# Kernel optimization log

Measured on AMD Instinct MI355X. Metric: run time of the kernel, lower is better.

## Reference

```python
import math
import jax, jax.numpy as jnp
import numpy as np

B, I, D, H, K, MAXI, FF = 2, 1024, 1024, 16, 64, 1024, 4096
DH = D // H
EPS = 1e-5

def _ln(x, g, b):
    m = x.mean(-1, keepdims=True)
    v = ((x - m) ** 2).mean(-1, keepdims=True)
    return (x - m) / jnp.sqrt(v + EPS) * g + b

def setup_inputs() -> dict:
    key = jax.random.key(0)
    ks = jax.random.split(key, 16)
    p = lambda i, sh: (0.02 * jax.random.normal(ks[i], sh)).astype(jnp.float32)
    # clamped relative-position indices: clamp(j - floor(1.0*i), -K, K) + K
    ar = np.arange(MAXI)
    idx = np.clip(ar[None, :] - ar[:, None], -K, K) + K  # [maxI, maxI]
    return {
        'x': jax.random.normal(ks[0], (B, I, D), dtype=jnp.float32),
        'j': jax.random.normal(ks[1], (B, I, D), dtype=jnp.float32),
        'ln1_g': jnp.ones((D,), jnp.float32), 'ln1_b': jnp.zeros((D,), jnp.float32),
        'Wv_w': p(2, (D, D)), 'Wv_b': jnp.zeros((D,), jnp.float32),
        'Wg_w': p(3, (D, D)), 'Wg_b': jnp.zeros((D,), jnp.float32),
        'lnv_g': jnp.ones((D,), jnp.float32), 'lnv_b': jnp.zeros((D,), jnp.float32),
        'Wq1_w': p(4, (D, D)), 'Wq1_b': jnp.zeros((D,), jnp.float32),
        'Wk_w': p(5, (D, D)), 'Wk_b': jnp.zeros((D,), jnp.float32),
        'Wq2_w': p(6, (D, D)), 'Wq2_b': jnp.zeros((D,), jnp.float32),
        'rel_emb': p(7, (2 * K + 1, D)),
        'Wo_w': p(8, (D, D)), 'Wo_b': jnp.zeros((D,), jnp.float32),
        'ln2_g': jnp.ones((D,), jnp.float32), 'ln2_b': jnp.zeros((D,), jnp.float32),
        'ff1_w': p(9, (D, FF)), 'ff1_b': jnp.zeros((FF,), jnp.float32),
        'ff2_w': p(10, (FF, D)), 'ff2_b': jnp.zeros((D,), jnp.float32),
        'indices': jnp.asarray(idx, jnp.int32),
    }

def reference(x, j, ln1_g, ln1_b, Wv_w, Wv_b, Wg_w, Wg_b, lnv_g, lnv_b,
              Wq1_w, Wq1_b, Wk_w, Wk_b, Wq2_w, Wq2_b, rel_emb,
              Wo_w, Wo_b, ln2_g, ln2_b, ff1_w, ff1_b, ff2_w, ff2_b, indices):
    Bv, Iq, _ = x.shape
    res = x
    xn = _ln(x, ln1_g, ln1_b)
    # value / gate streams with gelu activation, layernorm on v only
    v = _ln(jax.nn.gelu(xn @ Wv_w + Wv_b, approximate=False), lnv_g, lnv_b)
    g = jax.nn.gelu(xn @ Wg_w + Wg_b, approximate=False)
    vh = v.reshape(Bv, -1, H, DH)   # [B,J,H,Dh]
    gh = g.reshape(Bv, -1, H, DH)   # [B,I,H,Dh]
    # absolute-position scores: Q1(j) . K(j)^T
    q1 = (j @ Wq1_w + Wq1_b).reshape(Bv, -1, H, DH)
    kh = (j @ Wk_w + Wk_b).reshape(Bv, -1, H, DH)
    aa = jnp.einsum('bihd,bjhd->bhij', q1, kh)  # [B,H,I,J]
    # relative-position scores: Q2(j) . rel_embed^T, gathered by clamped indices
    q2 = (j @ Wq2_w + Wq2_b).reshape(Bv, -1, H, DH)
    rh = rel_emb.reshape(2 * K + 1, H, DH)
    arf = jnp.einsum('bihd,rhd->bhir', q2, rh)  # [B,H,I,2K+1]
    Jk = kh.shape[1]
    idx = jnp.broadcast_to(indices[None, None, :Iq, :Jk], (Bv, H, Iq, Jk))
    ar = jnp.take_along_axis(arf, idx, axis=-1)  # [B,H,I,J]
    a = jax.nn.softmax((aa + ar) / math.sqrt(DH), axis=-1)
    o = jnp.einsum('bhij,bjhd->bihd', a, vh) * gh  # gated attention output
    o = o.reshape(Bv, -1, D) @ Wo_w + Wo_b
    x1 = o + res
    # feed-forward sublayer
    h = jax.nn.relu(_ln(x1, ln2_g, ln2_b) @ ff1_w + ff1_b)
    out = h @ ff2_w + ff2_b + x1
    return (out, a)
```

## Files before the change

kernel.cpp:

```cpp
#include <hip/hip_runtime.h>
#include <hip/hip_bf16.h>
#include <math.h>

#define D_   1024
#define H_   16
#define DH_  64
#define FF_  4096
#define R_   129
#define I_   1024
#define B_   2
#define MROWS 2048
#define QKVLD 3072

typedef __bf16 v8bf16 __attribute__((ext_vector_type(8)));
typedef float f32x4 __attribute__((ext_vector_type(4)));

__device__ __forceinline__ float gelu_f(float x) {
    return 0.5f * x * (1.0f + erff(x * 0.7071067811865476f));
}

__device__ __forceinline__ void ldsld16(const void* g, void* l) {
    __builtin_amdgcn_global_load_lds(
        (const __attribute__((address_space(1))) void*)g,
        (__attribute__((address_space(3))) void*)l, 16, 0, 0);
}

__global__ __launch_bounds__(256) void cvt_bf16(const float* __restrict__ in,
        __hip_bfloat16* __restrict__ out, int n4) {
    int i = blockIdx.x * 256 + threadIdx.x;
    if (i >= n4) return;
    float4 v = reinterpret_cast<const float4*>(in)[i];
    union { __hip_bfloat16 h[4]; uint2 u; } pk;
    pk.h[0] = __float2bfloat16(v.x); pk.h[1] = __float2bfloat16(v.y);
    pk.h[2] = __float2bfloat16(v.z); pk.h[3] = __float2bfloat16(v.w);
    reinterpret_cast<uint2*>(out)[i] = pk.u;
}

__global__ __launch_bounds__(256) void wtrans(const float* __restrict__ W,
        __hip_bfloat16* __restrict__ WT, int K, int N) {
    __shared__ float T[64][65];
    int k0 = blockIdx.y * 64, n0 = blockIdx.x * 64;
    int t = threadIdx.x;
#pragma unroll
    for (int i = 0; i < 16; i++) {
        int e = t + i * 256, r = e >> 6, c = e & 63;
        T[r][c] = W[(size_t)(k0 + r) * N + n0 + c];
    }
    __syncthreads();
#pragma unroll
    for (int i = 0; i < 16; i++) {
        int e = t + i * 256, r = e >> 6, c = e & 63;
        WT[(size_t)(n0 + r) * K + k0 + c] = __float2bfloat16(T[c][r]);
    }
}

__global__ __launch_bounds__(256) void wtrans6(
        const float* __restrict__ s0, const float* __restrict__ s1,
        const float* __restrict__ s2, const float* __restrict__ s3,
        const float* __restrict__ s4, const float* __restrict__ s5,
        __hip_bfloat16* __restrict__ d0, __hip_bfloat16* __restrict__ d1,
        __hip_bfloat16* __restrict__ d2, __hip_bfloat16* __restrict__ d3,
        __hip_bfloat16* __restrict__ d4, __hip_bfloat16* __restrict__ d5) {
    __shared__ float T[64][65];
    int z = blockIdx.z;
    const float* W = z == 0 ? s0 : z == 1 ? s1 : z == 2 ? s2 : z == 3 ? s3 : z == 4 ? s4 : s5;
    __hip_bfloat16* WT = z == 0 ? d0 : z == 1 ? d1 : z == 2 ? d2 : z == 3 ? d3 : z == 4 ? d4 : d5;
    int k0 = blockIdx.y * 64, n0 = blockIdx.x * 64;
    int t = threadIdx.x;
#pragma unroll
    for (int i = 0; i < 16; i++) {
        int e = t + i * 256, r = e >> 6, c = e & 63;
        T[r][c] = W[(size_t)(k0 + r) * D_ + n0 + c];
    }
    __syncthreads();
#pragma unroll
    for (int i = 0; i < 16; i++) {
        int e = t + i * 256, r = e >> 6, c = e & 63;
        WT[(size_t)(n0 + r) * D_ + k0 + c] = __float2bfloat16(T[c][r]);
    }
}

__global__ __launch_bounds__(256) void vtrans(const float* __restrict__ v,
        __hip_bfloat16* __restrict__ vt) {
    __shared__ float T[64][65];
    int z = blockIdx.y, b = z >> 4, h = z & 15;
    int j0 = blockIdx.x * 64;
    int t = threadIdx.x;
#pragma unroll
    for (int i = 0; i < 16; i++) {
        int e = t + i * 256, r = e >> 6, c = e & 63;
        T[r][c] = v[(size_t)(b * I_ + j0 + r) * D_ + h * DH_ + c];
    }
    __syncthreads();
#pragma unroll
    for (int i = 0; i < 16; i++) {
        int e = t + i * 256, r = e >> 6, c = e & 63;
        vt[((size_t)z * DH_ + r) * I_ + j0 + c] = __float2bfloat16(T[c][r]);
    }
}

template<int MR, int NWC, int ACT, int RES, int OUTBF>
__global__ __launch_bounds__(256) void gemm_mfma(
        const __hip_bfloat16* __restrict__ A,
        const __hip_bfloat16* __restrict__ Bt,
        const float* __restrict__ bias,
        const float* __restrict__ res,
        void* __restrict__ Cout,
        int N, int Kd, int lda, int ldb, int ldc,
        size_t sAb, size_t sAh, size_t sBb, size_t sBh, size_t sCz) {
    constexpr int NWR = 4 / NWC;
    constexpr int BM = NWR * MR * 16;
    constexpr int BN = NWC * 64;
    __shared__ __align__(16) __hip_bfloat16 As[BM * 64];
    __shared__ __align__(16) __hip_bfloat16 Bs[BN * 64];
    const char* AsB = (const char*)As;
    const char* BsB = (const char*)Bs;
    int z = blockIdx.z;
    const __hip_bfloat16* Ab = A + (size_t)(z >> 4) * sAb + (size_t)(z & 15) * sAh;
    const __hip_bfloat16* Bb = Bt + (size_t)(z >> 4) * sBb + (size_t)(z & 15) * sBh;
    float* Cf = (float*)Cout + (size_t)z * sCz;
    __hip_bfloat16* Cb = (__hip_bfloat16*)Cout + (size_t)z * sCz;
    int m0 = blockIdx.y * BM, n0 = blockIdx.x * BN;
    int t = threadIdx.x;
    int l = t & 63, w = t >> 6;
    int wr = w / NWC, wc = w % NWC;
    int lr = l & 15, kq = l >> 4;
    int rx = lr & 7;

    f32x4 acc[MR][4] = {};

    for (int k0 = 0; k0 < Kd; k0 += 64) {
#pragma unroll
        for (int i = 0; i < BM / 32; i++) {
            int e = t + i * 256;
            int row = e >> 3, sl = e & 7;
            int kb = sl ^ (row & 7);
            ldsld16(Ab + (size_t)(m0 + row) * lda + (k0 + kb * 8), (void*)(AsB + e * 16));
        }
#pragma unroll
        for (int i = 0; i < BN / 32; i++) {
            int e = t + i * 256;
            int row = e >> 3, sl = e & 7;
            int kb = sl ^ (row & 7);
            int nr = n0 + row; if (nr > N - 1) nr = N - 1;
            ldsld16(Bb + (size_t)nr * ldb + (k0 + kb * 8), (void*)(BsB + e * 16));
        }
        __syncthreads();
#pragma unroll
        for (int kc = 0; kc < 2; kc++) {
            int sloff = (((kc << 2) + kq) ^ rx) << 4;
            v8bf16 af[MR], bfr[4];
#pragma unroll
            for (int mr = 0; mr < MR; mr++)
                af[mr] = *(const v8bf16*)(AsB + ((wr * (MR * 16) + mr * 16 + lr) << 7) + sloff);
#pragma unroll
            for (int nc = 0; nc < 4; nc++)
                bfr[nc] = *(const v8bf16*)(BsB + ((wc * 64 + nc * 16 + lr) << 7) + sloff);
#pragma unroll
            for (int mr = 0; mr < MR; mr++)
#pragma unroll
                for (int nc = 0; nc < 4; nc++)
                    acc[mr][nc] = __builtin_amdgcn_mfma_f32_16x16x32_bf16(
                        af[mr], bfr[nc], acc[mr][nc], 0, 0, 0);
        }
        __syncthreads();
    }

#pragma unroll
    for (int mr = 0; mr < MR; mr++) {
        int rbase = m0 + wr * (MR * 16) + mr * 16 + kq * 4;
#pragma unroll
        for (int nc = 0; nc < 4; nc++) {
            int col = n0 + wc * 64 + nc * 16 + lr;
            bool okc = col < N;
            float bv = (bias && okc) ? bias[col] : 0.f;
#pragma unroll
            for (int ri = 0; ri < 4; ri++) {
                int r = rbase + ri;
                float val = acc[mr][nc][ri] + bv;
                if (ACT == 1) val = gelu_f(val);
                if (ACT == 2) val = fmaxf(val, 0.f);
                if (RES) val += res[(size_t)r * ldc + col];
                if (okc) {
                    if (OUTBF == 2) {
                        if (col < D_) Cf[(size_t)r * ldc + col] = val;
                        else ((__hip_bfloat16*)res)[(size_t)r * ldc + (col - D_)] =
                                 __float2bfloat16(val);
                    } else if (OUTBF == 1) {
                        Cb[(size_t)r * ldc + col] = __float2bfloat16(val);
                    } else {
                        Cf[(size_t)r * ldc + col] = val;
                    }
                }
            }
        }
    }
}

#define FA_AR 0
#define FA_K  16896
#define FA_V  (16896 + 8192)
#define FA_P  (16896 + 16384)
#define SC2   0.1803368801111244f
__global__ __launch_bounds__(256) void flash_attn3(
        const __hip_bfloat16* __restrict__ qkv,
        const __hip_bfloat16* __restrict__ vt,
        const __hip_bfloat16* __restrict__ arfb,
        const __hip_bfloat16* __restrict__ gb,
        float* __restrict__ a_out,
        __hip_bfloat16* __restrict__ obuf) {
    __shared__ __align__(16) char lds[16896 + 8192 * 3];
    __hip_bfloat16* arl = (__hip_bfloat16*)(lds + FA_AR);
    char* kB = lds + FA_K;
    char* vB = lds + FA_V;
    char* pB = lds + FA_P;

    int z = blockIdx.y, b = z >> 4, h = z & 15;
    int i0 = blockIdx.x * 64;
    int t = threadIdx.x, l = t & 63, w = t >> 6;
    int lr = l & 15, kq = l >> 4;

#pragma unroll
    for (int i = 0; i < 2; i++) {
        int e = t + i * 256;
        int row = e >> 3, sl = e & 7;
        int kb = sl ^ (row & 7);
        ldsld16(qkv + (size_t)(b * I_ + i0 + row) * QKVLD + h * DH_ + kb * 8,
                (void*)(pB + e * 16));
    }
    for (int idx = t; idx < 64 * 132; idx += 256) {
        int row = idx / 132, r = idx - row * 132;
        if (r < R_) arl[idx] = arfb[((size_t)z * I_ + i0 + row) * R_ + r];
    }
    __syncthreads();
    v8bf16 qf[2];
#pragma unroll
    for (int kc = 0; kc < 2; kc++)
        qf[kc] = *(const v8bf16*)(pB + ((w * 16 + lr) << 7) + ((((kc << 2) + kq) ^ (lr & 7)) << 4));

    int irow = w * 16 + kq * 4;
    int ig = i0 + irow;
    float loS[4], hiS[4];
#pragma unroll
    for (int ri = 0; ri < 4; ri++) {
        loS[ri] = __bfloat162float(arl[(irow + ri) * 132 + 0])   * SC2;
        hiS[ri] = __bfloat162float(arl[(irow + ri) * 132 + 128]) * SC2;
    }

    float l_ln[4] = {0.f, 0.f, 0.f, 0.f};
    for (int jt = 0; jt < 16; jt++) {
        int j0 = jt * 64;
#pragma unroll
        for (int i = 0; i < 2; i++) {
            int e = t + i * 256;
            int row = e >> 3, sl = e & 7;
            int kb = sl ^ (row & 7);
            ldsld16(qkv + (size_t)(b * I_ + j0 + row) * QKVLD + D_ + h * DH_ + kb * 8,
                    (void*)(kB + e * 16));
        }
        __syncthreads();
        f32x4 acc[4] = {};
        __builtin_amdgcn_s_setprio(1);
#pragma unroll
        for (int kc = 0; kc < 2; kc++) {
            int sloff = ((((kc << 2) + kq)) ^ (lr & 7)) << 4;
#pragma unroll
            for (int tt = 0; tt < 4; tt++) {
                v8bf16 kf = *(const v8bf16*)(kB + ((tt * 16 + lr) << 7) + sloff);
                acc[tt] = __builtin_amdgcn_mfma_f32_16x16x32_bf16(qf[kc], kf, acc[tt], 0, 0, 0);
            }
        }
        __builtin_amdgcn_s_setprio(0);
#pragma unroll
        for (int ri = 0; ri < 4; ri++) {
            int i_g = ig + ri;
            float sc[4];
            bool lo_all = (j0 + 63) <= (i_g - 64);
            bool hi_all = j0 >= (i_g + 64);
            if (lo_all || hi_all) {
                float c = lo_all ? loS[ri] : hiS[ri];
#pragma unroll
                for (int tt = 0; tt < 4; tt++) sc[tt] = fmaf(acc[tt][ri], SC2, c);
            } else {
#pragma unroll
                for (int tt = 0; tt < 4; tt++) {
                    int rel = j0 + tt * 16 + lr - i_g;
                    rel = rel < -64 ? -64 : (rel > 64 ? 64 : rel);
                    sc[tt] = (acc[tt][ri] + __bfloat162float(arl[(irow + ri) * 132 + rel + 64])) * SC2;
                }
            }
            l_ln[ri] += exp2f(sc[0]) + exp2f(sc[1]) + exp2f(sc[2]) + exp2f(sc[3]);
        }
        __syncthreads();
    }
    float offb[4];
#pragma unroll
    for (int ri = 0; ri < 4; ri++) {
        float s = l_ln[ri];
#pragma unroll
        for (int off = 1; off < 16; off <<= 1) s += __shfl_xor(s, off, 64);
        offb[ri] = __log2f(s);
    }

    f32x4 oacc[4] = {};
    for (int jt = 0; jt < 16; jt++) {
        int j0 = jt * 64;
#pragma unroll
        for (int i = 0; i < 2; i++) {
            int e = t + i * 256;
            int row = e >> 3, sl = e & 7;
            int kb = sl ^ (row & 7);
            ldsld16(qkv + (size_t)(b * I_ + j0 + row) * QKVLD + D_ + h * DH_ + kb * 8,
                    (void*)(kB + e * 16));
            ldsld16(vt + ((size_t)z * DH_ + row) * I_ + j0 + kb * 8,
                    (void*)(vB + e * 16));
        }
        __syncthreads();
        f32x4 acc[4] = {};
        __builtin_amdgcn_s_setprio(1);
#pragma unroll
        for (int kc = 0; kc < 2; kc++) {
            int sloff = ((((kc << 2) + kq)) ^ (lr & 7)) << 4;
#pragma unroll
            for (int tt = 0; tt < 4; tt++) {
                v8bf16 kf = *(const v8bf16*)(kB + ((tt * 16 + lr) << 7) + sloff);
                acc[tt] = __builtin_amdgcn_mfma_f32_16x16x32_bf16(qf[kc], kf, acc[tt], 0, 0, 0);
            }
        }
        __builtin_amdgcn_s_setprio(0);
#pragma unroll
        for (int ri = 0; ri < 4; ri++) {
            int i_g = ig + ri;
            int rowl = irow + ri;
            float sc[4];
            bool lo_all = (j0 + 63) <= (i_g - 64);
            bool hi_all = j0 >= (i_g + 64);
            if (lo_all || hi_all) {
                float c = lo_all ? loS[ri] : hiS[ri];
#pragma unroll
                for (int tt = 0; tt < 4; tt++) sc[tt] = fmaf(acc[tt][ri], SC2, c);
            } else {
#pragma unroll
                for (int tt = 0; tt < 4; tt++) {
                    int rel = j0 + tt * 16 + lr - i_g;
                    rel = rel < -64 ? -64 : (rel > 64 ? 64 : rel);
                    sc[tt] = (acc[tt][ri] + __bfloat162float(arl[rowl * 132 + rel + 64])) * SC2;
                }
            }
            float* gout = a_out + ((size_t)z * I_ + i0 + rowl) * I_ + j0;
#pragma unroll
            for (int tt = 0; tt < 4; tt++) {
                float p = exp2f(sc[tt] - offb[ri]);
                __builtin_nontemporal_store(p, gout + tt * 16 + lr);
                *(__hip_bfloat16*)(pB + (rowl << 7) +
                        ((((tt * 2) + (lr >> 3)) ^ (rowl & 7)) << 4) + (lr & 7) * 2) =
                    __float2bfloat16(p);
            }
        }
        __syncthreads();
        __builtin_amdgcn_s_setprio(1);
#pragma unroll
        for (int kc = 0; kc < 2; kc++) {
            int sloff = ((((kc << 2) + kq)) ^ (lr & 7)) << 4;
            v8bf16 pf = *(const v8bf16*)(pB + ((w * 16 + lr) << 7) + sloff);
#pragma unroll
            for (int nc = 0; nc < 4; nc++) {
                v8bf16 vf = *(const v8bf16*)(vB + ((nc * 16 + lr) << 7) + sloff);
                oacc[nc] = __builtin_amdgcn_mfma_f32_16x16x32_bf16(pf, vf, oacc[nc], 0, 0, 0);
            }
        }
        __builtin_amdgcn_s_setprio(0);
        __syncthreads();
    }
#pragma unroll
    for (int nc = 0; nc < 4; nc++) {
#pragma unroll
        for (int ri = 0; ri < 4; ri++) {
            int r = i0 + irow + ri;
            size_t oi = ((size_t)(b * I_ + r)) * D_ + h * DH_ + nc * 16 + lr;
            obuf[oi] = __float2bfloat16(oacc[nc][ri] * __bfloat162float(gb[oi]));
        }
    }
}

template<int OUTBF>
__global__ __launch_bounds__(256) void ln_kernel(const float* __restrict__ in,
        void* __restrict__ out, const float* __restrict__ gw,
        const float* __restrict__ bw) {
    __shared__ float shs[4], shq[4];
    int row = blockIdx.x;
    int t = threadIdx.x;
    float4 v = reinterpret_cast<const float4*>(in + (size_t)row * D_)[t];
    float s = v.x + v.y + v.z + v.w;
#pragma unroll
    for (int off = 32; off > 0; off >>= 1) s += __shfl_down(s, off, 64);
    if ((t & 63) == 0) shs[t >> 6] = s;
    __syncthreads();
    float mean = (shs[0] + shs[1] + shs[2] + shs[3]) * (1.0f / D_);
    float d0 = v.x - mean, d1 = v.y - mean, d2 = v.z - mean, d3 = v.w - mean;
    float q = d0 * d0 + d1 * d1 + d2 * d2 + d3 * d3;
#pragma unroll
    for (int off = 32; off > 0; off >>= 1) q += __shfl_down(q, off, 64);
    if ((t & 63) == 0) shq[t >> 6] = q;
    __syncthreads();
    float var = (shq[0] + shq[1] + shq[2] + shq[3]) * (1.0f / D_);
    float rstd = rsqrtf(var + 1e-5f);
    float4 g4 = reinterpret_cast<const float4*>(gw)[t];
    float4 b4 = reinterpret_cast<const float4*>(bw)[t];
    float o0 = d0 * rstd * g4.x + b4.x;
    float o1 = d1 * rstd * g4.y + b4.y;
    float o2 = d2 * rstd * g4.z + b4.z;
    float o3 = d3 * rstd * g4.w + b4.w;
    if (OUTBF) {
        union { __hip_bfloat16 h[4]; uint2 u; } pk;
        pk.h[0] = __float2bfloat16(o0); pk.h[1] = __float2bfloat16(o1);
        pk.h[2] = __float2bfloat16(o2); pk.h[3] = __float2bfloat16(o3);
        reinterpret_cast<uint2*>((__hip_bfloat16*)out + (size_t)row * D_)[t] = pk.u;
    } else {
        float4 o; o.x = o0; o.y = o1; o.z = o2; o.w = o3;
        reinterpret_cast<float4*>((float*)out + (size_t)row * D_)[t] = o;
    }
}

extern "C" void kernel_launch(void* const* d_in, const int* in_sizes, int n_in,
                              void* d_out, int out_size, void* d_ws, size_t ws_size,
                              hipStream_t stream) {
    const float* x      = (const float*)d_in[0];
    const float* jin    = (const float*)d_in[1];
    const float* ln1_g  = (const float*)d_in[2];
    const float* ln1_b  = (const float*)d_in[3];
    const float* Wv_w   = (const float*)d_in[4];
    const float* Wv_b   = (const float*)d_in[5];
    const float* Wg_w   = (const float*)d_in[6];
    const float* Wg_b   = (const float*)d_in[7];
    const float* lnv_g  = (const float*)d_in[8];
    const float* lnv_b  = (const float*)d_in[9];
    const float* Wq1_w  = (const float*)d_in[10];
    const float* Wq1_b  = (const float*)d_in[11];
    const float* Wk_w   = (const float*)d_in[12];
    const float* Wk_b   = (const float*)d_in[13];
    const float* Wq2_w  = (const float*)d_in[14];
    const float* Wq2_b  = (const float*)d_in[15];
    const float* rel    = (const float*)d_in[16];
    const float* Wo_w   = (const float*)d_in[17];
    const float* Wo_b   = (const float*)d_in[18];
    const float* ln2_g  = (const float*)d_in[19];
    const float* ln2_b  = (const float*)d_in[20];
    const float* ff1_w  = (const float*)d_in[21];
    const float* ff1_b  = (const float*)d_in[22];
    const float* ff2_w  = (const float*)d_in[23];
    const float* ff2_b  = (const float*)d_in[24];

    float* out0  = (float*)d_out;
    float* a_out = out0 + (size_t)B_ * I_ * D_;

    char* wsb = (char*)d_ws;
    const size_t MB = 1u << 20;
    __hip_bfloat16* wvwgT= (__hip_bfloat16*)(wsb + 0 * MB);
    __hip_bfloat16* qkvT = (__hip_bfloat16*)(wsb + 4 * MB);
    __hip_bfloat16* WoT  = (__hip_bfloat16*)(wsb + 10 * MB);
    __hip_bfloat16* ff1T = (__hip_bfloat16*)(wsb + 12 * MB);
    __hip_bfloat16* ff2T = (__hip_bfloat16*)(wsb + 20 * MB);
    __hip_bfloat16* jbf  = (__hip_bfloat16*)(wsb + 28 * MB);
    __hip_bfloat16* qkv  = (__hip_bfloat16*)(wsb + 32 * MB);
    __hip_bfloat16* relb = (__hip_bfloat16*)(wsb + 44 * MB);
    __hip_bfloat16* arfb = (__hip_bfloat16*)(wsb + 45 * MB);
    __hip_bfloat16* gbuf = (__hip_bfloat16*)(wsb + 54 * MB);
    float*          vbuf = (float*)        (wsb + 58 * MB);
    __hip_bfloat16* xnb  = (__hip_bfloat16*)(wsb + 28 * MB);
    __hip_bfloat16* vt   = (__hip_bfloat16*)(wsb + 28 * MB);
    __hip_bfloat16* obuf = (__hip_bfloat16*)(wsb + 58 * MB);
    float*          x1   = (float*)        (wsb + 32 * MB);
    __hip_bfloat16* x1nb = (__hip_bfloat16*)(wsb + 40 * MB);
    __hip_bfloat16* hbuf = (__hip_bfloat16*)(wsb + 44 * MB);
    float*          bias3= (float*)        (wsb + 66 * MB);
    float*          bias2= (float*)        (wsb + 66 * MB + 16384);

    dim3 blk(256);

    cvt_bf16<<<2048, blk, 0, stream>>>(jin, jbf, (MROWS * D_) / 4);
    cvt_bf16<<<129, blk, 0, stream>>>(rel, relb, (R_ * D_) / 4);
    hipMemcpyAsync(bias3,        Wq1_b, D_ * 4, hipMemcpyDeviceToDevice, stream);
    hipMemcpyAsync(bias3 + D_,   Wk_b,  D_ * 4, hipMemcpyDeviceToDevice, stream);
    hipMemcpyAsync(bias3 + 2*D_, Wq2_b, D_ * 4, hipMemcpyDeviceToDevice, stream);
    hipMemcpyAsync(bias2,        Wv_b,  D_ * 4, hipMemcpyDeviceToDevice, stream);
    hipMemcpyAsync(bias2 + D_,   Wg_b,  D_ * 4, hipMemcpyDeviceToDevice, stream);
    wtrans6<<<dim3(16, 16, 6), blk, 0, stream>>>(
        Wq1_w, Wk_w, Wq2_w, Wv_w, Wg_w, Wo_w,
        qkvT, qkvT + 1024*1024, qkvT + 2048*1024,
        wvwgT, wvwgT + 1024*1024, WoT);
    wtrans<<<dim3(64, 16), blk, 0, stream>>>(ff1_w, ff1T, D_, FF_);
    wtrans<<<dim3(16, 64), blk, 0, stream>>>(ff2_w, ff2T, FF_, D_);

    gemm_mfma<2, 2, 0, 0, 1><<<dim3(24, 32, 1), blk, 0, stream>>>(
        jbf, qkvT, bias3, nullptr, qkv, QKVLD, D_, D_, D_, QKVLD, 0, 0, 0, 0, 0);
    gemm_mfma<4, 2, 0, 0, 1><<<dim3(2, 8, 32), blk, 0, stream>>>(
        qkv + 2 * D_, relb, nullptr, nullptr, arfb,
        R_, DH_, QKVLD, D_, R_,
        (size_t)I_ * QKVLD, (size_t)DH_, 0, (size_t)DH_, (size_t)I_ * R_);

    ln_kernel<1><<<MROWS, blk, 0, stream>>>(x, xnb, ln1_g, ln1_b);
    gemm_mfma<2, 2, 1, 0, 2><<<dim3(16, 32, 1), blk, 0, stream>>>(
        xnb, wvwgT, bias2, (const float*)gbuf, vbuf, 2 * D_, D_, D_, D_, D_, 0, 0, 0, 0, 0);
    ln_kernel<0><<<MROWS, blk, 0, stream>>>(vbuf, vbuf, lnv_g, lnv_b);
    vtrans<<<dim3(16, 32), blk, 0, stream>>>(vbuf, vt);

    flash_attn3<<<dim3(16, 32), blk, 0, stream>>>(qkv, vt, arfb, gbuf, a_out, obuf);

    gemm_mfma<2, 1, 0, 1, 0><<<dim3(16, 16, 1), blk, 0, stream>>>(
        obuf, WoT, Wo_b, x, x1, D_, D_, D_, D_, D_, 0, 0, 0, 0, 0);
    ln_kernel<1><<<MROWS, blk, 0, stream>>>(x1, x1nb, ln2_g, ln2_b);
    gemm_mfma<4, 2, 2, 0, 1><<<dim3(32, 16, 1), blk, 0, stream>>>(
        x1nb, ff1T, ff1_b, nullptr, hbuf, FF_, D_, D_, D_, FF_, 0, 0, 0, 0, 0);
    gemm_mfma<2, 1, 0, 1, 0><<<dim3(16, 16, 1), blk, 0, stream>>>(
        hbuf, ff2T, ff2_b, x1, out0, D_, FF_, FF_, FF_, D_, 0, 0, 0, 0, 0);
}
```

Before: 281.1 us.

## Merge small setup launches and enlarge M-tiles for QKV and value/gate GEMMs

Replaces the rel_emb conversion and five bias memcpys with one combined kernel, and merges the two FF weight transposes into a single launch. This cuts the number of launches and memcpy operations. It also switches the QKV and value/gate GEMMs to a taller M tile (4 instead of 2) with half as many row blocks, which improves operand reuse but leaves fewer workgroups to fill the CUs.

```diff
diff --git a/kernel.cpp b/kernel.cpp
--- a/kernel.cpp
+++ b/kernel.cpp
@@ -36,21 +36,25 @@
     reinterpret_cast<uint2*>(out)[i] = pk.u;
 }
 
-__global__ __launch_bounds__(256) void wtrans(const float* __restrict__ W,
-        __hip_bfloat16* __restrict__ WT, int K, int N) {
-    __shared__ float T[64][65];
-    int k0 = blockIdx.y * 64, n0 = blockIdx.x * 64;
-    int t = threadIdx.x;
-#pragma unroll
-    for (int i = 0; i < 16; i++) {
-        int e = t + i * 256, r = e >> 6, c = e & 63;
-        T[r][c] = W[(size_t)(k0 + r) * N + n0 + c];
-    }
-    __syncthreads();
-#pragma unroll
-    for (int i = 0; i < 16; i++) {
-        int e = t + i * 256, r = e >> 6, c = e & 63;
-        WT[(size_t)(n0 + r) * K + k0 + c] = __float2bfloat16(T[c][r]);
+__global__ __launch_bounds__(256) void cvt_rel_bias(const float* __restrict__ rel,
+        __hip_bfloat16* __restrict__ relb,
+        const float* __restrict__ q1b_, const float* __restrict__ kb_,
+        const float* __restrict__ q2b_, const float* __restrict__ vb_,
+        const float* __restrict__ gb_,
+        float* __restrict__ bias3, float* __restrict__ bias2) {
+    int bid = blockIdx.x, t = threadIdx.x;
+    if (bid < 129) {
+        int i = bid * 256 + t;
+        float4 v = reinterpret_cast<const float4*>(rel)[i];
+        union { __hip_bfloat16 h[4]; uint2 u; } pk;
+        pk.h[0] = __float2bfloat16(v.x); pk.h[1] = __float2bfloat16(v.y);
+        pk.h[2] = __float2bfloat16(v.z); pk.h[3] = __float2bfloat16(v.w);
+        reinterpret_cast<uint2*>(relb)[i] = pk.u;
+    } else {
+        int k = bid - 129;
+        const float* src = k == 0 ? q1b_ : k == 1 ? kb_ : k == 2 ? q2b_ : k == 3 ? vb_ : gb_;
+        float* dst = (k < 3 ? bias3 + k * D_ : bias2 + (k - 3) * D_);
+        reinterpret_cast<float4*>(dst)[t] = reinterpret_cast<const float4*>(src)[t];
     }
 }
 
@@ -77,6 +81,31 @@
     for (int i = 0; i < 16; i++) {
         int e = t + i * 256, r = e >> 6, c = e & 63;
         WT[(size_t)(n0 + r) * D_ + k0 + c] = __float2bfloat16(T[c][r]);
+    }
+}
+
+__global__ __launch_bounds__(256) void wtrans_ff(
+        const float* __restrict__ f1, const float* __restrict__ f2,
+        __hip_bfloat16* __restrict__ d1, __hip_bfloat16* __restrict__ d2) {
+    __shared__ float T[64][65];
+    int z = blockIdx.z;
+    const float* W = z == 0 ? f1 : f2;
+    __hip_bfloat16* WT = z == 0 ? d1 : d2;
+    int K = z == 0 ? D_ : FF_;
+    int N = z == 0 ? FF_ : D_;
+    int k0 = (z == 0 ? blockIdx.y : blockIdx.x) * 64;
+    int n0 = (z == 0 ? blockIdx.x : blockIdx.y) * 64;
+    int t = threadIdx.x;
+#pragma unroll
+    for (int i = 0; i < 16; i++) {
+        int e = t + i * 256, r = e >> 6, c = e & 63;
+        T[r][c] = W[(size_t)(k0 + r) * N + n0 + c];
+    }
+    __syncthreads();
+#pragma unroll
+    for (int i = 0; i < 16; i++) {
+        int e = t + i * 256, r = e >> 6, c = e & 63;
+        WT[(size_t)(n0 + r) * K + k0 + c] = __float2bfloat16(T[c][r]);
     }
 }
 
@@ -479,20 +508,15 @@
     dim3 blk(256);
 
     cvt_bf16<<<2048, blk, 0, stream>>>(jin, jbf, (MROWS * D_) / 4);
-    cvt_bf16<<<129, blk, 0, stream>>>(rel, relb, (R_ * D_) / 4);
-    hipMemcpyAsync(bias3,        Wq1_b, D_ * 4, hipMemcpyDeviceToDevice, stream);
-    hipMemcpyAsync(bias3 + D_,   Wk_b,  D_ * 4, hipMemcpyDeviceToDevice, stream);
-    hipMemcpyAsync(bias3 + 2*D_, Wq2_b, D_ * 4, hipMemcpyDeviceToDevice, stream);
-    hipMemcpyAsync(bias2,        Wv_b,  D_ * 4, hipMemcpyDeviceToDevice, stream);
-    hipMemcpyAsync(bias2 + D_,   Wg_b,  D_ * 4, hipMemcpyDeviceToDevice, stream);
+    cvt_rel_bias<<<134, blk, 0, stream>>>(rel, relb,
+        Wq1_b, Wk_b, Wq2_b, Wv_b, Wg_b, bias3, bias2);
     wtrans6<<<dim3(16, 16, 6), blk, 0, stream>>>(
         Wq1_w, Wk_w, Wq2_w, Wv_w, Wg_w, Wo_w,
         qkvT, qkvT + 1024*1024, qkvT + 2048*1024,
         wvwgT, wvwgT + 1024*1024, WoT);
-    wtrans<<<dim3(64, 16), blk, 0, stream>>>(ff1_w, ff1T, D_, FF_);
-    wtrans<<<dim3(16, 64), blk, 0, stream>>>(ff2_w, ff2T, FF_, D_);
-
-    gemm_mfma<2, 2, 0, 0, 1><<<dim3(24, 32, 1), blk, 0, stream>>>(
+    wtrans_ff<<<dim3(64, 16, 2), blk, 0, stream>>>(ff1_w, ff2_w, ff1T, ff2T);
+
+    gemm_mfma<4, 2, 0, 0, 1><<<dim3(24, 16, 1), blk, 0, stream>>>(
         jbf, qkvT, bias3, nullptr, qkv, QKVLD, D_, D_, D_, QKVLD, 0, 0, 0, 0, 0);
     gemm_mfma<4, 2, 0, 0, 1><<<dim3(2, 8, 32), blk, 0, stream>>>(
         qkv + 2 * D_, relb, nullptr, nullptr, arfb,
@@ -500,7 +524,7 @@
         (size_t)I_ * QKVLD, (size_t)DH_, 0, (size_t)DH_, (size_t)I_ * R_);
 
     ln_kernel<1><<<MROWS, blk, 0, stream>>>(x, xnb, ln1_g, ln1_b);
-    gemm_mfma<2, 2, 1, 0, 2><<<dim3(16, 32, 1), blk, 0, stream>>>(
+    gemm_mfma<4, 2, 1, 0, 2><<<dim3(16, 16, 1), blk, 0, stream>>>(
         xnb, wvwgT, bias2, (const float*)gbuf, vbuf, 2 * D_, D_, D_, D_, D_, 0, 0, 0, 0, 0);
     ln_kernel<0><<<MROWS, blk, 0, stream>>>(vbuf, vbuf, lnv_g, lnv_b);
     vtrans<<<dim3(16, 32), blk, 0, stream>>>(vbuf, vt);
```

Measured after the change: 288.3 us. +2.5%, slower.
